# Kernel optimization log

Measured on AMD Instinct MI355X. Metric: run time of the kernel, lower is better.

The kernel has to match this reference:

```python
import jax, jax.numpy as jnp
import numpy as np

N, D, DH, H = 2048, 256, 256, 4
DHEAD = DH // H
NEG = -1e30


def setup_inputs() -> dict:
    key = jax.random.key(0)
    ks = jax.random.split(key, 24)
    s = 0.05
    inp = {
        'axiom_states': jax.random.normal(ks[0], (N, D), jnp.float32),
        'adj0': (jax.random.uniform(ks[1], (N, N)) < 0.015).astype(jnp.float32),
        'adj1': (jax.random.uniform(ks[2], (N, N)) < 0.015).astype(jnp.float32),
        'w0': jax.random.uniform(ks[3], (N, N), jnp.float32),
        'w1': jax.random.uniform(ks[4], (N, N), jnp.float32),
        'Wm0': jax.random.normal(ks[5], (DH, D), jnp.float32) * s,
        'bm0': jax.random.normal(ks[6], (DH,), jnp.float32) * s,
        'Wa0': jax.random.normal(ks[7], (H, 2 * D), jnp.float32) * s,
        'ba0': jax.random.normal(ks[8], (H,), jnp.float32) * s,
        'Wm1': jax.random.normal(ks[9], (DH, D), jnp.float32) * s,
        'bm1': jax.random.normal(ks[10], (DH,), jnp.float32) * s,
        'Wa1': jax.random.normal(ks[11], (H, 2 * D), jnp.float32) * s,
        'ba1': jax.random.normal(ks[12], (H,), jnp.float32) * s,
        'gru_wih': jax.random.normal(ks[13], (3 * D, 2 * DH), jnp.float32) * s,
        'gru_whh': jax.random.normal(ks[14], (3 * D, D), jnp.float32) * s,
        'gru_bih': jax.random.normal(ks[15], (3 * D,), jnp.float32) * s,
        'gru_bhh': jax.random.normal(ks[16], (3 * D,), jnp.float32) * s,
        'ln_g': jnp.ones((D,), jnp.float32),
        'ln_b': jnp.zeros((D,), jnp.float32),
    }
    return inp


def _edge_messages(x, adj, w, Wm, bm, Wa, ba):
    # GAT-style decomposition of Linear([x_i, x_j]) -> a_cur[i] + a_nb[j] + b
    a_cur = x @ Wa[:, :D].T                      # [N,H] (target i, first half of concat)
    a_nb = x @ Wa[:, D:].T                       # [N,H] (neighbor j, second half)
    s = a_nb[:, None, :] + a_cur[None, :, :] + ba  # [j,i,H]
    s = jax.nn.leaky_relu(s, 0.2)
    s = s * w[:, :, None]                        # edge-weight scaled scores (pre-softmax)
    mask = adj != 0                              # edge j -> i iff adj[j,i] != 0
    logits = jnp.where(mask[:, :, None], s, NEG)
    attn = jax.nn.softmax(logits, axis=0) * mask[:, :, None]  # zero for isolated nodes
    msg = (x @ Wm.T + bm).reshape(N, H, DHEAD)   # per-neighbor messages
    agg = jnp.einsum('jih,jhd->ihd', attn, msg)  # softmax-weighted sum over neighbors
    return agg.reshape(N, DH)


def _forward(axiom_states, adj0, adj1, w0, w1, Wm0, bm0, Wa0, ba0,
             Wm1, bm1, Wa1, ba1, gru_wih, gru_whh, gru_bih, gru_bhh, ln_g, ln_b):
    m0 = _edge_messages(axiom_states, adj0, w0, Wm0, bm0, Wa0, ba0)
    m1 = _edge_messages(axiom_states, adj1, w1, Wm1, bm1, Wa1, ba1)
    msg = jnp.concatenate([m0, m1], axis=-1)     # dropout is identity in eval
    # GRUCell (torch semantics)
    gi = msg @ gru_wih.T + gru_bih
    gh = axiom_states @ gru_whh.T + gru_bhh
    r = jax.nn.sigmoid(gi[:, :D] + gh[:, :D])
    z = jax.nn.sigmoid(gi[:, D:2 * D] + gh[:, D:2 * D])
    n = jnp.tanh(gi[:, 2 * D:] + r * gh[:, 2 * D:])
    h = (1.0 - z) * n + z * axiom_states
    # LayerNorm
    mu = jnp.mean(h, axis=-1, keepdims=True)
    var = jnp.var(h, axis=-1, keepdims=True)
    return (h - mu) * jax.lax.rsqrt(var + 1e-5) * ln_g + ln_b


def reference(axiom_states, adj0, adj1, w0, w1, Wm0, bm0, Wa0, ba0,
              Wm1, bm1, Wa1, ba1, gru_wih, gru_whh, gru_bih, gru_bhh, ln_g, ln_b):
    return _forward(axiom_states, adj0, adj1, w0, w1, Wm0, bm0, Wa0, ba0,
                    Wm1, bm1, Wa1, ba1, gru_wih, gru_whh, gru_bih, gru_bhh, ln_g, ln_b)
```

## Files before the change

kernel.cpp:

```cpp
#include <hip/hip_runtime.h>

#define NN 2048
#define DD 256
#define HH 4
#define ECAP 128

typedef unsigned short ushort_t;
typedef __attribute__((ext_vector_type(4))) unsigned short us4;
typedef __attribute__((ext_vector_type(8))) unsigned short us8;
typedef __attribute__((ext_vector_type(8))) short s8;
typedef __attribute__((ext_vector_type(4))) float f4;

__device__ __forceinline__ ushort_t f2b(float f) {
    unsigned int u = __float_as_uint(f);
    return (ushort_t)((u + 0x7fffu + ((u >> 16) & 1u)) >> 16);
}
__device__ __forceinline__ float b2f(ushort_t b) {
    return __uint_as_float(((unsigned int)b) << 16);
}
__device__ __forceinline__ void gl_lds16(const void* g, void* l) {
    __builtin_amdgcn_global_load_lds(
        (const __attribute__((address_space(1))) void*)g,
        (__attribute__((address_space(3))) void*)l, 16, 0, 0);
}

__device__ __forceinline__ void gemm_core(
    const ushort_t* __restrict__ A, int lda, const ushort_t* __restrict__ B, int ldb,
    int r0, int c0, int K, ushort_t (*as)[64], ushort_t (*bs)[64], f4 acc[2][2])
{
    const int t = threadIdx.x;
    const int wave = t >> 6, lane = t & 63;
    const int wm = (wave & 1) * 32, wn = (wave >> 1) * 32;
    const int fm = lane & 15, fq = lane >> 4;

    const int m0q0 = wave * 16 + (lane >> 3);
    const int m0q1 = m0q0 + 8;
    const int cs0 = ((lane & 7) ^ (m0q0 & 7)) * 8;
    const int cs1 = ((lane & 7) ^ (m0q1 & 7)) * 8;
    const ushort_t* ga0 = A + (size_t)(r0 + m0q0) * lda + cs0;
    const ushort_t* ga1 = A + (size_t)(r0 + m0q1) * lda + cs1;
    const ushort_t* gb0 = B + (size_t)(c0 + m0q0) * ldb + cs0;
    const ushort_t* gb1 = B + (size_t)(c0 + m0q1) * ldb + cs1;
    ushort_t* la0 = &as[wave * 16][0];
    ushort_t* la1 = &as[wave * 16 + 8][0];
    ushort_t* lb0 = &bs[wave * 16][0];
    ushort_t* lb1 = &bs[wave * 16 + 8][0];
    const int ra0 = wm + fm, ra1 = wm + 16 + fm;
    const int rb0 = wn + fm, rb1 = wn + 16 + fm;

    for (int k0 = 0; k0 < K; k0 += 64) {
        __syncthreads();
        gl_lds16(ga0 + k0, la0);
        gl_lds16(ga1 + k0, la1);
        gl_lds16(gb0 + k0, lb0);
        gl_lds16(gb1 + k0, lb1);
        __syncthreads();
        #pragma unroll
        for (int kk = 0; kk < 2; ++kk) {
            const int cc = kk * 4 + fq;
            const s8 a0 = *(const s8*)&as[ra0][(cc ^ (ra0 & 7)) * 8];
            const s8 a1 = *(const s8*)&as[ra1][(cc ^ (ra1 & 7)) * 8];
            const s8 b0 = *(const s8*)&bs[rb0][(cc ^ (rb0 & 7)) * 8];
            const s8 b1 = *(const s8*)&bs[rb1][(cc ^ (rb1 & 7)) * 8];
            acc[0][0] = __builtin_amdgcn_mfma_f32_16x16x32_bf16(a0, b0, acc[0][0], 0, 0, 0);
            acc[0][1] = __builtin_amdgcn_mfma_f32_16x16x32_bf16(a0, b1, acc[0][1], 0, 0, 0);
            acc[1][0] = __builtin_amdgcn_mfma_f32_16x16x32_bf16(a1, b0, acc[1][0], 0, 0, 0);
            acc[1][1] = __builtin_amdgcn_mfma_f32_16x16x32_bf16(a1, b1, acc[1][1], 0, 0, 0);
        }
    }
}

__device__ __forceinline__ us8 cvt8(float4 a, float4 b) {
    us8 o;
    o[0] = f2b(a.x); o[1] = f2b(a.y); o[2] = f2b(a.z); o[3] = f2b(a.w);
    o[4] = f2b(b.x); o[5] = f2b(b.y); o[6] = f2b(b.z); o[7] = f2b(b.w);
    return o;
}

__device__ __forceinline__ void gemm_core_f32(
    const float* __restrict__ A, int lda, const float* __restrict__ B, int ldb,
    int r0, int c0, int K, ushort_t (*as)[64], ushort_t (*bs)[64], f4 acc[2][2])
{
    const int t = threadIdx.x;
    const int wave = t >> 6, lane = t & 63;
    const int wm = (wave & 1) * 32, wn = (wave >> 1) * 32;
    const int fm = lane & 15, fq = lane >> 4;

    const int m1 = wave * 16 + (lane >> 3);
    const int m2 = m1 + 8;
    const int g1 = ((lane & 7) ^ (m1 & 7)) * 8;
    const int g2 = ((lane & 7) ^ (m2 & 7)) * 8;
    const int cl = (lane & 7) * 8;
    const int ra0 = wm + fm, ra1 = wm + 16 + fm;
    const int rb0 = wn + fm, rb1 = wn + 16 + fm;

    for (int k0 = 0; k0 < K; k0 += 64) {
        const float4 aa0 = *(const float4*)(A + (size_t)(r0 + m1) * lda + k0 + g1);
        const float4 aa1 = *(const float4*)(A + (size_t)(r0 + m1) * lda + k0 + g1 + 4);
        const float4 ab0 = *(const float4*)(A + (size_t)(r0 + m2) * lda + k0 + g2);
        const float4 ab1 = *(const float4*)(A + (size_t)(r0 + m2) * lda + k0 + g2 + 4);
        const float4 ba0 = *(const float4*)(B + (size_t)(c0 + m1) * ldb + k0 + g1);
        const float4 ba1 = *(const float4*)(B + (size_t)(c0 + m1) * ldb + k0 + g1 + 4);
        const float4 bb0 = *(const float4*)(B + (size_t)(c0 + m2) * ldb + k0 + g2);
        const float4 bb1 = *(const float4*)(B + (size_t)(c0 + m2) * ldb + k0 + g2 + 4);
        __syncthreads();
        *(us8*)&as[m1][cl] = cvt8(aa0, aa1);
        *(us8*)&as[m2][cl] = cvt8(ab0, ab1);
        *(us8*)&bs[m1][cl] = cvt8(ba0, ba1);
        *(us8*)&bs[m2][cl] = cvt8(bb0, bb1);
        __syncthreads();
        #pragma unroll
        for (int kk = 0; kk < 2; ++kk) {
            const int cc = kk * 4 + fq;
            const s8 a0 = *(const s8*)&as[ra0][(cc ^ (ra0 & 7)) * 8];
            const s8 a1 = *(const s8*)&as[ra1][(cc ^ (ra1 & 7)) * 8];
            const s8 b0 = *(const s8*)&bs[rb0][(cc ^ (rb0 & 7)) * 8];
            const s8 b1 = *(const s8*)&bs[rb1][(cc ^ (rb1 & 7)) * 8];
            acc[0][0] = __builtin_amdgcn_mfma_f32_16x16x32_bf16(a0, b0, acc[0][0], 0, 0, 0);
            acc[0][1] = __builtin_amdgcn_mfma_f32_16x16x32_bf16(a0, b1, acc[0][1], 0, 0, 0);
            acc[1][0] = __builtin_amdgcn_mfma_f32_16x16x32_bf16(a1, b0, acc[1][0], 0, 0, 0);
            acc[1][1] = __builtin_amdgcn_mfma_f32_16x16x32_bf16(a1, b1, acc[1][1], 0, 0, 0);
        }
    }
}

#define E_SC  256
#define E_AP  384
#define E_WI  768
#define E_NB  1408

__global__ __launch_bounds__(256) void fused1_kernel(
    const float* __restrict__ x,
    const float* __restrict__ adj0, const float* __restrict__ adj1,
    const float* __restrict__ Wm0, const float* __restrict__ Wm1,
    const float* __restrict__ whh, const float* __restrict__ wih,
    const float* __restrict__ Wa0, const float* __restrict__ Wa1,
    const float* __restrict__ bm0, const float* __restrict__ bm1,
    const float* __restrict__ bhh,
    int* __restrict__ cnt, int* __restrict__ ej,
    ushort_t* __restrict__ wihb,
    float* __restrict__ acur, float* __restrict__ anb,
    ushort_t* __restrict__ msgb, float* __restrict__ gh)
{
    __shared__ char smem[16448];
    const int b = blockIdx.x, t = threadIdx.x;

    if (b < E_SC) {
        const int l = b & 1, chunk = b >> 1;
        const int i0 = chunk * 16;
        const float* adj = l ? adj1 : adj0;
        int* lcnt = (int*)smem;
        if (t < 16) lcnt[t] = 0;
        __syncthreads();
        const int rowLane = t >> 2, q = t & 3;
        for (int r0r = 0; r0r < NN; r0r += 512) {
            float4 a[8];
            #pragma unroll
            for (int it = 0; it < 8; ++it) {
                const int j = r0r + it * 64 + rowLane;
                a[it] = *(const float4*)(adj + (size_t)j * NN + i0 + q * 4);
            }
            #pragma unroll
            for (int it = 0; it < 8; ++it) {
                const int j = r0r + it * 64 + rowLane;
                const float av[4] = {a[it].x, a[it].y, a[it].z, a[it].w};
                #pragma unroll
                for (int u = 0; u < 4; ++u) {
                    if (av[u] != 0.f) {
                        const int li = q * 4 + u;
                        const int slot = atomicAdd(&lcnt[li], 1);
                        if (slot < ECAP)
                            ej[((size_t)l * NN + i0 + li) * ECAP + slot] = j;
                    }
                }
            }
        }
        __syncthreads();
        if (t < 16) cnt[l * NN + i0 + t] = min(lcnt[t], ECAP);
        return;
    }
    if (b < E_AP) {
        float* sh = (float*)smem;
        const int i0 = (b - E_SC) * 16;
        for (int rr = 0; rr < 16; ++rr)
            sh[rr * 257 + t] = x[(size_t)(i0 + rr) * DD + t];
        __syncthreads();
        const int r = t >> 4, idx = t & 15;
        const int l = idx >> 3, isnb = (idx >> 2) & 1, h = idx & 3;
        const float* wrow = (l ? Wa1 : Wa0) + h * (2 * DD) + isnb * DD;
        float acc = 0.f;
        for (int k = 0; k < DD; ++k) acc = fmaf(sh[r * 257 + k], wrow[k], acc);
        float* dst = isnb ? anb : acur;
        dst[((size_t)l * NN + i0 + r) * HH + h] = acc;
        return;
    }
    if (b < E_WI) {
        const int id = (b - E_AP) * 1024 + t * 4;
        const float4 v = *(const float4*)(wih + id);
        us4 o; o.x = f2b(v.x); o.y = f2b(v.y); o.z = f2b(v.z); o.w = f2b(v.w);
        *(us4*)(wihb + id) = o;
        return;
    }
    {
        ushort_t (*as)[64] = (ushort_t(*)[64])smem;
        ushort_t (*bs)[64] = (ushort_t(*)[64])(smem + 8192);
        const int wave = t >> 6, lane = t & 63;
        const int wm = (wave & 1) * 32, wn = (wave >> 1) * 32;
        const int fm = lane & 15, fq = lane >> 4;
        const int idx = b - E_WI;
        const int c0 = (idx % 20) * 64, r0 = (idx / 20) * 64;
        const float* Bsrc = (c0 < 256) ? Wm0 + (size_t)c0 * DD
                          : (c0 < 512) ? Wm1 + (size_t)(c0 - 256) * DD
                                       : whh + (size_t)(c0 - 512) * DD;
        f4 acc[2][2] = {};
        gemm_core_f32(x, DD, Bsrc, DD, r0, 0, DD, as, bs, acc);
        #pragma unroll
        for (int ni = 0; ni < 2; ++ni) {
            const int col = c0 + wn + ni * 16 + fm;
            const float bv = (col < 256) ? bm0[col]
                           : (col < 512) ? bm1[col - 256]
                                         : bhh[col - 512];
            #pragma unroll
            for (int mi = 0; mi < 2; ++mi) {
                #pragma unroll
                for (int r = 0; r < 4; ++r) {
                    const int row = r0 + wm + mi * 16 + fq * 4 + r;
                    const float v = acc[mi][ni][r] + bv;
                    if (col < 512) msgb[(size_t)row * 512 + col] = f2b(v);
                    else           gh[(size_t)row * 768 + col - 512] = v;
                }
            }
        }
    }
}

__global__ __launch_bounds__(256) void attn_kernel(
    const int* __restrict__ cnt, const int* __restrict__ ej,
    const float* __restrict__ w0, const float* __restrict__ w1,
    const float* __restrict__ acur, const float* __restrict__ anb,
    const float* __restrict__ ba0, const float* __restrict__ ba1,
    const ushort_t* __restrict__ msgb, ushort_t* __restrict__ mcatb)
{
    const int i = blockIdx.x, l = blockIdx.y, t = threadIdx.x;
    __shared__ float es[HH][ECAP];
    __shared__ int ejs[ECAP];
    const int ne = min(max(cnt[l * NN + i], 0), ECAP);
    const float* ba = l ? ba1 : ba0;
    const float* w  = l ? w1 : w0;
    const size_t ebase = ((size_t)l * NN + i) * ECAP;

    if (t < ne) {
        const int j = ej[ebase + t];
        const float wv = w[(size_t)j * NN + i];
        ejs[t] = j;
        const float4 av = *(const float4*)(anb + ((size_t)l * NN + j) * HH);
        const float sv[4] = {av.x, av.y, av.z, av.w};
        #pragma unroll
        for (int h = 0; h < HH; ++h) {
            float s = sv[h] + acur[((size_t)l * NN + i) * HH + h] + ba[h];
            s = (s > 0.f) ? s : 0.2f * s;
            es[h][t] = s * wv;
        }
    }
    __syncthreads();
    {
        const int h = t >> 6, lane = t & 63;
        float s0 = (lane < ne) ? es[h][lane] : -1e30f;
        float s1 = (lane + 64 < ne) ? es[h][lane + 64] : -1e30f;
        float m = fmaxf(s0, s1);
        #pragma unroll
        for (int off = 32; off; off >>= 1) m = fmaxf(m, __shfl_xor(m, off));
        const float p0 = expf(s0 - m), p1 = expf(s1 - m);
        float sum = p0 + p1;
        #pragma unroll
        for (int off = 32; off; off >>= 1) sum += __shfl_xor(sum, off);
        const float inv = (ne > 0) ? 1.f / sum : 0.f;
        es[h][lane] = p0 * inv;
        if (lane + 64 < ECAP) es[h][lane + 64] = p1 * inv;
    }
    __syncthreads();
    const int h = t >> 6;
    const int off = l * DD + t;
    float acc = 0.f;
    int e = 0;
    for (; e + 4 <= ne; e += 4) {
        const float v0 = b2f(msgb[(size_t)ejs[e + 0] * 512 + off]);
        const float v1 = b2f(msgb[(size_t)ejs[e + 1] * 512 + off]);
        const float v2 = b2f(msgb[(size_t)ejs[e + 2] * 512 + off]);
        const float v3 = b2f(msgb[(size_t)ejs[e + 3] * 512 + off]);
        acc = fmaf(es[h][e + 0], v0, acc);
        acc = fmaf(es[h][e + 1], v1, acc);
        acc = fmaf(es[h][e + 2], v2, acc);
        acc = fmaf(es[h][e + 3], v3, acc);
    }
    for (; e < ne; ++e)
        acc = fmaf(es[h][e], b2f(msgb[(size_t)ejs[e] * 512 + off]), acc);
    mcatb[(size_t)i * (2 * DD) + off] = f2b(acc);
}

__global__ __launch_bounds__(256) void gemm2_kernel(
    const ushort_t* __restrict__ mcatb, const ushort_t* __restrict__ wihb,
    const float* __restrict__ bih, float* __restrict__ gi)
{
    __shared__ ushort_t as[64][64];
    __shared__ ushort_t bs[64][64];
    const int t = threadIdx.x;
    const int wave = t >> 6, lane = t & 63;
    const int wm = (wave & 1) * 32, wn = (wave >> 1) * 32;
    const int fm = lane & 15, fq = lane >> 4;
    const int c0 = blockIdx.x * 64, r0 = blockIdx.y * 64;
    f4 acc[2][2] = {};
    gemm_core(mcatb, 512, wihb, 512, r0, c0, 512, as, bs, acc);
    #pragma unroll
    for (int ni = 0; ni < 2; ++ni) {
        const int col = c0 + wn + ni * 16 + fm;
        const float bv = bih[col];
        #pragma unroll
        for (int mi = 0; mi < 2; ++mi)
            #pragma unroll
            for (int r = 0; r < 4; ++r)
                gi[(size_t)(r0 + wm + mi * 16 + fq * 4 + r) * 768 + col] =
                    acc[mi][ni][r] + bv;
    }
}

__global__ __launch_bounds__(256) void gates_ln(
    const float* __restrict__ gi, const float* __restrict__ gh, const float* __restrict__ x,
    const float* __restrict__ lng, const float* __restrict__ lnb, float* __restrict__ out)
{
    __shared__ float rs1[4], rs2[4];
    const int t = threadIdx.x;
    const int r0 = blockIdx.x * 4;
    const float gv = lng[t], bv = lnb[t];
    float hv[4];
    #pragma unroll
    for (int r = 0; r < 4; ++r) {
        const int row = r0 + r;
        const float gir = gi[(size_t)row * 768 + t];
        const float giz = gi[(size_t)row * 768 + 256 + t];
        const float gin = gi[(size_t)row * 768 + 512 + t];
        const float ghr = gh[(size_t)row * 768 + t];
        const float ghz = gh[(size_t)row * 768 + 256 + t];
        const float ghn = gh[(size_t)row * 768 + 512 + t];
        const float rr = 1.f / (1.f + expf(-(gir + ghr)));
        const float zz = 1.f / (1.f + expf(-(giz + ghz)));
        const float nn = tanhf(gin + rr * ghn);
        hv[r] = (1.f - zz) * nn + zz * x[(size_t)row * DD + t];
    }
    const int lane = t & 63, wid = t >> 6;
    for (int r = 0; r < 4; ++r) {
        float s1 = hv[r], s2 = hv[r] * hv[r];
        #pragma unroll
        for (int off = 32; off; off >>= 1) {
            s1 += __shfl_down(s1, off);
            s2 += __shfl_down(s2, off);
        }
        if (lane == 0) { rs1[wid] = s1; rs2[wid] = s2; }
        __syncthreads();
        const float sum = rs1[0] + rs1[1] + rs1[2] + rs1[3];
        const float sq  = rs2[0] + rs2[1] + rs2[2] + rs2[3];
        const float mu  = sum * (1.f / DD);
        const float var = sq * (1.f / DD) - mu * mu;
        const float inv = rsqrtf(var + 1e-5f);
        out[(size_t)(r0 + r) * DD + t] = (hv[r] - mu) * inv * gv + bv;
        __syncthreads();
    }
}

extern "C" void kernel_launch(void* const* d_in, const int* in_sizes, int n_in,
                              void* d_out, int out_size, void* d_ws, size_t ws_size,
                              hipStream_t stream)
{
    const float* x    = (const float*)d_in[0];
    const float* adj0 = (const float*)d_in[1];
    const float* adj1 = (const float*)d_in[2];
    const float* w0   = (const float*)d_in[3];
    const float* w1   = (const float*)d_in[4];
    const float* Wm0  = (const float*)d_in[5];
    const float* bm0  = (const float*)d_in[6];
    const float* Wa0  = (const float*)d_in[7];
    const float* ba0  = (const float*)d_in[8];
    const float* Wm1  = (const float*)d_in[9];
    const float* bm1  = (const float*)d_in[10];
    const float* Wa1  = (const float*)d_in[11];
    const float* ba1  = (const float*)d_in[12];
    const float* wih  = (const float*)d_in[13];
    const float* whh  = (const float*)d_in[14];
    const float* bih  = (const float*)d_in[15];
    const float* bhh  = (const float*)d_in[16];
    const float* lng  = (const float*)d_in[17];
    const float* lnb  = (const float*)d_in[18];
    float* out = (float*)d_out;

    float* ws = (float*)d_ws;
    float* gh   = ws;            ws += (size_t)NN * 768;
    float* gi   = ws;            ws += (size_t)NN * 768;
    float* acur = ws;            ws += 2 * NN * HH;
    float* anb  = ws;            ws += 2 * NN * HH;
    int*   cnt  = (int*)ws;      ws += 2 * NN;
    int*   ej   = (int*)ws;      ws += 2 * NN * ECAP;
    ushort_t* wihb  = (ushort_t*)ws;  ws += (size_t)768 * 512 / 2;
    ushort_t* msgb  = (ushort_t*)ws;  ws += (size_t)NN * 512 / 2;
    ushort_t* mcatb = (ushort_t*)ws;  ws += (size_t)NN * 512 / 2;

    fused1_kernel<<<E_NB, 256, 0, stream>>>(
        x, adj0, adj1, Wm0, Wm1, whh, wih, Wa0, Wa1, bm0, bm1, bhh,
        cnt, ej, wihb, acur, anb, msgb, gh);
    attn_kernel<<<dim3(NN, 2), 256, 0, stream>>>(
        cnt, ej, w0, w1, acur, anb, ba0, ba1, msgb, mcatb);
    gemm2_kernel<<<dim3(12, 32), 256, 0, stream>>>(mcatb, wihb, bih, gi);
    gates_ln<<<NN / 4, 256, 0, stream>>>(gi, gh, x, lng, lnb, out);
}
```

Baseline: 167.8 us.

## Double-buffer GEMM tiles, prefetch f32 loads, widen gather unroll, wave-per-row LayerNorm

```diff
diff --git a/kernel.cpp b/kernel.cpp
--- a/kernel.cpp
+++ b/kernel.cpp
@@ -24,7 +24,7 @@
         (__attribute__((address_space(3))) void*)l, 16, 0, 0);
 }
 
-__device__ __forceinline__ void gemm_core(
+__device__ __forceinline__ void gemm_core_db(
     const ushort_t* __restrict__ A, int lda, const ushort_t* __restrict__ B, int ldb,
     int r0, int c0, int K, ushort_t (*as)[64], ushort_t (*bs)[64], f4 acc[2][2])
 {
@@ -41,32 +41,38 @@
     const ushort_t* ga1 = A + (size_t)(r0 + m0q1) * lda + cs1;
     const ushort_t* gb0 = B + (size_t)(c0 + m0q0) * ldb + cs0;
     const ushort_t* gb1 = B + (size_t)(c0 + m0q1) * ldb + cs1;
-    ushort_t* la0 = &as[wave * 16][0];
-    ushort_t* la1 = &as[wave * 16 + 8][0];
-    ushort_t* lb0 = &bs[wave * 16][0];
-    ushort_t* lb1 = &bs[wave * 16 + 8][0];
     const int ra0 = wm + fm, ra1 = wm + 16 + fm;
     const int rb0 = wn + fm, rb1 = wn + 16 + fm;
 
+    gl_lds16(ga0, &as[wave * 16][0]);
+    gl_lds16(ga1, &as[wave * 16 + 8][0]);
+    gl_lds16(gb0, &bs[wave * 16][0]);
+    gl_lds16(gb1, &bs[wave * 16 + 8][0]);
+    __syncthreads();
+
+    int buf = 0;
     for (int k0 = 0; k0 < K; k0 += 64) {
-        __syncthreads();
-        gl_lds16(ga0 + k0, la0);
-        gl_lds16(ga1 + k0, la1);
-        gl_lds16(gb0 + k0, lb0);
-        gl_lds16(gb1 + k0, lb1);
-        __syncthreads();
+        const int nb = buf ^ 64;
+        if (k0 + 64 < K) {
+            gl_lds16(ga0 + k0 + 64, &as[nb + wave * 16][0]);
+            gl_lds16(ga1 + k0 + 64, &as[nb + wave * 16 + 8][0]);
+            gl_lds16(gb0 + k0 + 64, &bs[nb + wave * 16][0]);
+            gl_lds16(gb1 + k0 + 64, &bs[nb + wave * 16 + 8][0]);
+        }
         #pragma unroll
         for (int kk = 0; kk < 2; ++kk) {
             const int cc = kk * 4 + fq;
-            const s8 a0 = *(const s8*)&as[ra0][(cc ^ (ra0 & 7)) * 8];
-            const s8 a1 = *(const s8*)&as[ra1][(cc ^ (ra1 & 7)) * 8];
-            const s8 b0 = *(const s8*)&bs[rb0][(cc ^ (rb0 & 7)) * 8];
-            const s8 b1 = *(const s8*)&bs[rb1][(cc ^ (rb1 & 7)) * 8];
+            const s8 a0 = *(const s8*)&as[buf + ra0][(cc ^ (ra0 & 7)) * 8];
+            const s8 a1 = *(const s8*)&as[buf + ra1][(cc ^ (ra1 & 7)) * 8];
+            const s8 b0 = *(const s8*)&bs[buf + rb0][(cc ^ (rb0 & 7)) * 8];
+            const s8 b1 = *(const s8*)&bs[buf + rb1][(cc ^ (rb1 & 7)) * 8];
             acc[0][0] = __builtin_amdgcn_mfma_f32_16x16x32_bf16(a0, b0, acc[0][0], 0, 0, 0);
             acc[0][1] = __builtin_amdgcn_mfma_f32_16x16x32_bf16(a0, b1, acc[0][1], 0, 0, 0);
             acc[1][0] = __builtin_amdgcn_mfma_f32_16x16x32_bf16(a1, b0, acc[1][0], 0, 0, 0);
             acc[1][1] = __builtin_amdgcn_mfma_f32_16x16x32_bf16(a1, b1, acc[1][1], 0, 0, 0);
         }
+        __syncthreads();
+        buf = nb;
     }
 }
 
@@ -94,21 +100,37 @@
     const int ra0 = wm + fm, ra1 = wm + 16 + fm;
     const int rb0 = wn + fm, rb1 = wn + 16 + fm;
 
+    const float* pa1 = A + (size_t)(r0 + m1) * lda + g1;
+    const float* pa2 = A + (size_t)(r0 + m2) * lda + g2;
+    const float* pb1 = B + (size_t)(c0 + m1) * ldb + g1;
+    const float* pb2 = B + (size_t)(c0 + m2) * ldb + g2;
+
+    float4 aa0 = *(const float4*)(pa1);
+    float4 aa1 = *(const float4*)(pa1 + 4);
+    float4 ab0 = *(const float4*)(pa2);
+    float4 ab1 = *(const float4*)(pa2 + 4);
+    float4 ba0 = *(const float4*)(pb1);
+    float4 ba1 = *(const float4*)(pb1 + 4);
+    float4 bb0 = *(const float4*)(pb2);
+    float4 bb1 = *(const float4*)(pb2 + 4);
+
     for (int k0 = 0; k0 < K; k0 += 64) {
-        const float4 aa0 = *(const float4*)(A + (size_t)(r0 + m1) * lda + k0 + g1);
-        const float4 aa1 = *(const float4*)(A + (size_t)(r0 + m1) * lda + k0 + g1 + 4);
-        const float4 ab0 = *(const float4*)(A + (size_t)(r0 + m2) * lda + k0 + g2);
-        const float4 ab1 = *(const float4*)(A + (size_t)(r0 + m2) * lda + k0 + g2 + 4);
-        const float4 ba0 = *(const float4*)(B + (size_t)(c0 + m1) * ldb + k0 + g1);
-        const float4 ba1 = *(const float4*)(B + (size_t)(c0 + m1) * ldb + k0 + g1 + 4);
-        const float4 bb0 = *(const float4*)(B + (size_t)(c0 + m2) * ldb + k0 + g2);
-        const float4 bb1 = *(const float4*)(B + (size_t)(c0 + m2) * ldb + k0 + g2 + 4);
         __syncthreads();
         *(us8*)&as[m1][cl] = cvt8(aa0, aa1);
         *(us8*)&as[m2][cl] = cvt8(ab0, ab1);
         *(us8*)&bs[m1][cl] = cvt8(ba0, ba1);
         *(us8*)&bs[m2][cl] = cvt8(bb0, bb1);
         __syncthreads();
+        if (k0 + 64 < K) {
+            aa0 = *(const float4*)(pa1 + k0 + 64);
+            aa1 = *(const float4*)(pa1 + k0 + 68);
+            ab0 = *(const float4*)(pa2 + k0 + 64);
+            ab1 = *(const float4*)(pa2 + k0 + 68);
+            ba0 = *(const float4*)(pb1 + k0 + 64);
+            ba1 = *(const float4*)(pb1 + k0 + 68);
+            bb0 = *(const float4*)(pb2 + k0 + 64);
+            bb1 = *(const float4*)(pb2 + k0 + 68);
+        }
         #pragma unroll
         for (int kk = 0; kk < 2; ++kk) {
             const int cc = kk * 4 + fq;
@@ -283,15 +305,14 @@
     const int off = l * DD + t;
     float acc = 0.f;
     int e = 0;
-    for (; e + 4 <= ne; e += 4) {
-        const float v0 = b2f(msgb[(size_t)ejs[e + 0] * 512 + off]);
-        const float v1 = b2f(msgb[(size_t)ejs[e + 1] * 512 + off]);
-        const float v2 = b2f(msgb[(size_t)ejs[e + 2] * 512 + off]);
-        const float v3 = b2f(msgb[(size_t)ejs[e + 3] * 512 + off]);
-        acc = fmaf(es[h][e + 0], v0, acc);
-        acc = fmaf(es[h][e + 1], v1, acc);
-        acc = fmaf(es[h][e + 2], v2, acc);
-        acc = fmaf(es[h][e + 3], v3, acc);
+    for (; e + 8 <= ne; e += 8) {
+        float v[8];
+        #pragma unroll
+        for (int u = 0; u < 8; ++u)
+            v[u] = b2f(msgb[(size_t)ejs[e + u] * 512 + off]);
+        #pragma unroll
+        for (int u = 0; u < 8; ++u)
+            acc = fmaf(es[h][e + u], v[u], acc);
     }
     for (; e < ne; ++e)
         acc = fmaf(es[h][e], b2f(msgb[(size_t)ejs[e] * 512 + off]), acc);
@@ -302,15 +323,15 @@
     const ushort_t* __restrict__ mcatb, const ushort_t* __restrict__ wihb,
     const float* __restrict__ bih, float* __restrict__ gi)
 {
-    __shared__ ushort_t as[64][64];
-    __shared__ ushort_t bs[64][64];
+    __shared__ ushort_t as[128][64];
+    __shared__ ushort_t bs[128][64];
     const int t = threadIdx.x;
     const int wave = t >> 6, lane = t & 63;
     const int wm = (wave & 1) * 32, wn = (wave >> 1) * 32;
     const int fm = lane & 15, fq = lane >> 4;
     const int c0 = blockIdx.x * 64, r0 = blockIdx.y * 64;
     f4 acc[2][2] = {};
-    gemm_core(mcatb, 512, wihb, 512, r0, c0, 512, as, bs, acc);
+    gemm_core_db(mcatb, 512, wihb, 512, r0, c0, 512, as, bs, acc);
     #pragma unroll
     for (int ni = 0; ni < 2; ++ni) {
         const int col = c0 + wn + ni * 16 + fm;
@@ -328,43 +349,45 @@
     const float* __restrict__ gi, const float* __restrict__ gh, const float* __restrict__ x,
     const float* __restrict__ lng, const float* __restrict__ lnb, float* __restrict__ out)
 {
-    __shared__ float rs1[4], rs2[4];
     const int t = threadIdx.x;
-    const int r0 = blockIdx.x * 4;
-    const float gv = lng[t], bv = lnb[t];
-    float hv[4];
+    const int lane = t & 63, wv = t >> 6;
+    const int row = blockIdx.x * 4 + wv;
+    const size_t b768 = (size_t)row * 768;
+    const int c = lane * 4;
+    const f4 gir = *(const f4*)(gi + b768 + c);
+    const f4 giz = *(const f4*)(gi + b768 + 256 + c);
+    const f4 gin = *(const f4*)(gi + b768 + 512 + c);
+    const f4 ghr = *(const f4*)(gh + b768 + c);
+    const f4 ghz = *(const f4*)(gh + b768 + 256 + c);
+    const f4 ghn = *(const f4*)(gh + b768 + 512 + c);
+    const f4 xv  = *(const f4*)(x + (size_t)row * DD + c);
+    f4 hv;
+    float s1 = 0.f, s2 = 0.f;
     #pragma unroll
-    for (int r = 0; r < 4; ++r) {
-        const int row = r0 + r;
-        const float gir = gi[(size_t)row * 768 + t];
-        const float giz = gi[(size_t)row * 768 + 256 + t];
-        const float gin = gi[(size_t)row * 768 + 512 + t];
-        const float ghr = gh[(size_t)row * 768 + t];
-        const float ghz = gh[(size_t)row * 768 + 256 + t];
-        const float ghn = gh[(size_t)row * 768 + 512 + t];
-        const float rr = 1.f / (1.f + expf(-(gir + ghr)));
-        const float zz = 1.f / (1.f + expf(-(giz + ghz)));
-        const float nn = tanhf(gin + rr * ghn);
-        hv[r] = (1.f - zz) * nn + zz * x[(size_t)row * DD + t];
-    }
-    const int lane = t & 63, wid = t >> 6;
-    for (int r = 0; r < 4; ++r) {
-        float s1 = hv[r], s2 = hv[r] * hv[r];
-        #pragma unroll
-        for (int off = 32; off; off >>= 1) {
-            s1 += __shfl_down(s1, off);
-            s2 += __shfl_down(s2, off);
-        }
-        if (lane == 0) { rs1[wid] = s1; rs2[wid] = s2; }
-        __syncthreads();
-        const float sum = rs1[0] + rs1[1] + rs1[2] + rs1[3];
-        const float sq  = rs2[0] + rs2[1] + rs2[2] + rs2[3];
-        const float mu  = sum * (1.f / DD);
-        const float var = sq * (1.f / DD) - mu * mu;
-        const float inv = rsqrtf(var + 1e-5f);
-        out[(size_t)(r0 + r) * DD + t] = (hv[r] - mu) * inv * gv + bv;
-        __syncthreads();
-    }
+    for (int u = 0; u < 4; ++u) {
+        const float rr = 1.f / (1.f + expf(-(gir[u] + ghr[u])));
+        const float zz = 1.f / (1.f + expf(-(giz[u] + ghz[u])));
+        const float nn = tanhf(gin[u] + rr * ghn[u]);
+        const float h = (1.f - zz) * nn + zz * xv[u];
+        hv[u] = h;
+        s1 += h;
+        s2 += h * h;
+    }
+    #pragma unroll
+    for (int off = 32; off; off >>= 1) {
+        s1 += __shfl_xor(s1, off);
+        s2 += __shfl_xor(s2, off);
+    }
+    const float mu  = s1 * (1.f / DD);
+    const float var = s2 * (1.f / DD) - mu * mu;
+    const float inv = rsqrtf(var + 1e-5f);
+    const f4 gv = *(const f4*)(lng + c);
+    const f4 bv = *(const f4*)(lnb + c);
+    f4 res;
+    #pragma unroll
+    for (int u = 0; u < 4; ++u)
+        res[u] = (hv[u] - mu) * inv * gv[u] + bv[u];
+    *(f4*)(out + (size_t)row * DD + c) = res;
 }
 
 extern "C" void kernel_launch(void* const* d_in, const int* in_sizes, int n_in,
```

New measurement: 167.6 us. About the same (-0.1%).
